# Optimization experiments

Measured on AMD Instinct MI355X. Metric: run time of the kernel, lower is better.

The kernel has to match this reference:

```python
import jax, jax.numpy as jnp
import numpy as np

N = 50000      # nodes
E = 800000     # edges
IN = 16        # embedding_dimension
HID = 128      # hidden_dimension
OUT = 3        # out_dim
R = 2          # relation_num
NEG_SLOPE = 0.2  # PyG RGATConv default negative_slope


def setup_inputs() -> dict:
    key = jax.random.key(0)
    ks = jax.random.split(key, 9)
    feature = jax.random.normal(ks[0], (N, IN), jnp.float32)
    edge_index = jax.random.randint(ks[1], (2, E), 0, N, jnp.int32)
    edge_type = jax.random.randint(ks[2], (E,), 0, R, jnp.int32)
    # RGATConv params (heads=1): weight [R, in, out], q/k [out, 1], bias [out]
    W1 = jax.random.normal(ks[3], (R, IN, HID), jnp.float32) * (1.0 / np.sqrt(IN))
    q1 = jax.random.normal(ks[4], (HID, 1), jnp.float32) * (1.0 / np.sqrt(HID))
    k1 = jax.random.normal(ks[5], (HID, 1), jnp.float32) * (1.0 / np.sqrt(HID))
    b1 = jnp.zeros((HID,), jnp.float32)
    W2 = jax.random.normal(ks[6], (R, HID, OUT), jnp.float32) * (1.0 / np.sqrt(HID))
    q2 = jax.random.normal(ks[7], (OUT, 1), jnp.float32) * (1.0 / np.sqrt(OUT))
    k2 = jax.random.normal(ks[8], (OUT, 1), jnp.float32) * (1.0 / np.sqrt(OUT))
    b2 = jnp.zeros((OUT,), jnp.float32)
    return dict(feature=feature, edge_index=edge_index, edge_type=edge_type,
                W1=W1, q1=q1, k1=k1, b1=b1, W2=W2, q2=q2, k2=k2, b2=b2)


def rgat_conv(x, src, dst, edge_type, W, q, k, b, n_nodes):
    # Per-relation node transform once at node level: [R, N, C]
    # (equivalent to per-edge bmm with W[edge_type] in PyG, but avoids
    #  gathering [E, in, C] weight matrices)
    xr = jnp.einsum('nd,rdc->rnc', x, W)
    out_i = xr[edge_type, dst]  # target node transformed by edge relation, [E, C]
    out_j = xr[edge_type, src]  # source node transformed by edge relation, [E, C]
    # additive self-attention, heads=1: alpha = leaky_relu(q(x_i) + k(x_j))
    alpha = jax.nn.leaky_relu((out_i @ q + out_j @ k)[:, 0], NEG_SLOPE)  # [E]
    # across-relation softmax over incoming edges of each target node
    m = jax.ops.segment_max(alpha, dst, num_segments=n_nodes)
    ex = jnp.exp(alpha - m[dst])
    denom = jax.ops.segment_sum(ex, dst, num_segments=n_nodes)
    a = ex / (denom[dst] + 1e-16)
    # message = alpha * W_r x_j, scatter-sum to target nodes
    out = jax.ops.segment_sum(out_j * a[:, None], dst, num_segments=n_nodes)
    return out + b


def reference(feature, edge_index, edge_type, W1, q1, k1, b1, W2, q2, k2, b2):
    src, dst = edge_index[0], edge_index[1]  # PyG: row 0 = source j, row 1 = target i
    h = rgat_conv(feature, src, dst, edge_type, W1, q1, k1, b1, N)
    # F.dropout(p=0.3) is identity in eval mode
    out = rgat_conv(h, src, dst, edge_type, W2, q2, k2, b2, N)
    return out
```

## Files before the change

### kernel.cpp

```cpp
#include <hip/hip_runtime.h>
#include <math.h>

#define IN_DIM 16
#define HID 128
#define NEG 0.2f

__device__ __forceinline__ float lrelu(float a) { return a > 0.f ? a : NEG * a; }

__global__ void __launch_bounds__(256) k_pre(
    const float* __restrict__ W1, const float* __restrict__ q1, const float* __restrict__ k1,
    const float* __restrict__ b1, const float* __restrict__ W2, const float* __restrict__ q2,
    const float* __restrict__ k2,
    float* __restrict__ wq1, float* __restrict__ wk1,
    float* __restrict__ M, float* __restrict__ C,
    int* __restrict__ counts, int n_nodes) {
    int zi = blockIdx.x * 256 + threadIdx.x;
    if (zi < n_nodes) counts[zi] = 0;

    int w = blockIdx.x * 4 + (threadIdx.x >> 6);
    if (w >= 362) return;
    int lane = threadIdx.x & 63;

    auto T = [&](int c, int o) -> float {
        if (o < 3) return W2[c * 3 + o];
        if (o < 6) return W2[384 + c * 3 + (o - 3)];
        const float* base = (o == 6 || o == 8) ? (W2 + c * 3) : (W2 + 384 + c * 3);
        const float* v = (o < 8) ? q2 : k2;
        return base[0] * v[0] + base[1] * v[1] + base[2] * v[2];
    };

    if (w < 330) {
        bool isC = (w >= 320);
        int o  = isC ? (w - 320) : (w % 10);
        int dp = isC ? 0 : (w / 10);
        float acc = 0.f;
        for (int c = lane; c < HID; c += 64) {
            float left = isC ? b1[c] : W1[dp * HID + c];
            acc += left * T(c, o);
        }
#pragma unroll
        for (int off = 32; off; off >>= 1) acc += __shfl_xor(acc, off);
        if (lane == 0) { if (isC) C[o] = acc; else M[dp * 10 + o] = acc; }
    } else {
        int i = w - 330;
        float aq = 0.f, ak = 0.f;
        for (int c = lane; c < HID; c += 64) {
            float wv = W1[i * HID + c];
            aq += wv * q1[c]; ak += wv * k1[c];
        }
#pragma unroll
        for (int off = 32; off; off >>= 1) { aq += __shfl_xor(aq, off); ak += __shfl_xor(ak, off); }
        if (lane == 0) { wq1[i] = aq; wk1[i] = ak; }
    }
}

__global__ void __launch_bounds__(256) k_prep(
    const float* __restrict__ x,
    const float* __restrict__ wq1, const float* __restrict__ wk1,
    float* __restrict__ sq1, float* __restrict__ sk1,
    const int* __restrict__ dstp, int* __restrict__ counts, int* __restrict__ rank,
    int n_nodes, int ecnt) {
    __shared__ float wq[2 * IN_DIM], wk[2 * IN_DIM];
    if (threadIdx.x < 2 * IN_DIM) { wq[threadIdx.x] = wq1[threadIdx.x]; wk[threadIdx.x] = wk1[threadIdx.x]; }
    __syncthreads();
    int gid = blockIdx.x * 256 + threadIdx.x;
    if (gid < ecnt) rank[gid] = atomicAdd(&counts[dstp[gid]], 1);
    if (gid < n_nodes) {
        float q0 = 0.f, q1v = 0.f, k0 = 0.f, k1v = 0.f;
        const float4* xp = reinterpret_cast<const float4*>(x + (size_t)gid * IN_DIM);
#pragma unroll
        for (int d4 = 0; d4 < IN_DIM / 4; ++d4) {
            float4 v = xp[d4];
            float vv[4] = {v.x, v.y, v.z, v.w};
#pragma unroll
            for (int j = 0; j < 4; ++j) {
                int d = d4 * 4 + j;
                q0 += vv[j] * wq[d]; q1v += vv[j] * wq[IN_DIM + d];
                k0 += vv[j] * wk[d]; k1v += vv[j] * wk[IN_DIM + d];
            }
        }
        sq1[gid] = q0; sq1[n_nodes + gid] = q1v;
        sk1[gid] = k0; sk1[n_nodes + gid] = k1v;
    }
}

__global__ void k_scan1(const int* __restrict__ counts, int* __restrict__ exoff,
                        int* __restrict__ blockSums, int n) {
    __shared__ int s[512];
    int tid = threadIdx.x;
    int gid = blockIdx.x * 512 + tid;
    int v = (gid < n) ? counts[gid] : 0;
    s[tid] = v;
    __syncthreads();
    for (int off = 1; off < 512; off <<= 1) {
        int t = (tid >= off) ? s[tid - off] : 0;
        __syncthreads();
        s[tid] += t;
        __syncthreads();
    }
    if (gid < n) exoff[gid] = s[tid] - v;
    if (tid == 511) blockSums[blockIdx.x] = s[511];
}

__global__ void __launch_bounds__(256) k_scatter(
    const int* __restrict__ srcp, const int* __restrict__ dstp,
    const int* __restrict__ etp,
    const int* __restrict__ exoff, const int* __restrict__ blockSums,
    const int* __restrict__ rank,
    int* __restrict__ offsets, int* __restrict__ sorted,
    int n_nodes, int ecnt, int nblk) {
    __shared__ int sB[128];
    int t = threadIdx.x;
    int v = 0;
    if (t < 128) { v = (t < nblk) ? blockSums[t] : 0; sB[t] = v; }
    __syncthreads();
    for (int off = 1; off < 128; off <<= 1) {
        int u = (t >= off && t < 128) ? sB[t - off] : 0;
        __syncthreads();
        if (t < 128) sB[t] += u;
        __syncthreads();
    }
    if (t < 128) sB[t] -= v;
    __syncthreads();
    int i = blockIdx.x * 256 + t;
    if (i < n_nodes) offsets[i] = exoff[i] + sB[i >> 9];
    if (i == 0) offsets[n_nodes] = ecnt;
    if (i < ecnt) {
        int d = dstp[i];
        int o = exoff[d] + sB[d >> 9];
        sorted[o + rank[i]] = (etp[i] << 16) | srcp[i];
    }
}

__global__ void __launch_bounds__(256) k_layer1(
    const int* __restrict__ offsets, const int* __restrict__ sorted,
    const float* __restrict__ sq1, const float* __restrict__ sk1,
    const float* __restrict__ x, const float* __restrict__ M, const float* __restrict__ C,
    float* __restrict__ xr2p, float* __restrict__ sq2,
    int n_nodes) {
    __shared__ float Ml[320], Cl[10];
    __shared__ float Al[4][32];
    for (int i = threadIdx.x; i < 320; i += 256) Ml[i] = M[i];
    if (threadIdx.x < 10)  Cl[threadIdx.x] = C[threadIdx.x];
    __syncthreads();
    int wid = threadIdx.x >> 6, lane = threadIdx.x & 63;
    int n = blockIdx.x * 4 + wid;
    if (n >= n_nodes) return;
    int beg = offsets[n], end = offsets[n + 1];
    float s0 = sq1[n], s1 = sq1[n_nodes + n];
    int ch4 = lane & 3, j = lane >> 2;
    float4 a0 = make_float4(0.f, 0.f, 0.f, 0.f);
    float4 a1 = make_float4(0.f, 0.f, 0.f, 0.f);
    float ds = 0.f;
    const float4* x4 = reinterpret_cast<const float4*>(x);
    for (int e = beg + j; e < end; e += 16) {
        int pk = sorted[e];
        int et = pk >> 16, s = pk & 0xFFFF;
        float w = __expf(lrelu((et ? s1 : s0) + sk1[et * n_nodes + s]));
        ds += w;
        float4 xv = x4[s * 4 + ch4];
        if (et == 0) { a0.x += w * xv.x; a0.y += w * xv.y; a0.z += w * xv.z; a0.w += w * xv.w; }
        else         { a1.x += w * xv.x; a1.y += w * xv.y; a1.z += w * xv.z; a1.w += w * xv.w; }
    }
#pragma unroll
    for (int off = 4; off <= 32; off <<= 1) {
        a0.x += __shfl_xor(a0.x, off); a0.y += __shfl_xor(a0.y, off);
        a0.z += __shfl_xor(a0.z, off); a0.w += __shfl_xor(a0.w, off);
        a1.x += __shfl_xor(a1.x, off); a1.y += __shfl_xor(a1.y, off);
        a1.z += __shfl_xor(a1.z, off); a1.w += __shfl_xor(a1.w, off);
        ds += __shfl_xor(ds, off);
    }
    float inv = 1.f / (ds + 1e-16f);
    if (lane < 4) {
        reinterpret_cast<float4*>(&Al[wid][0])[lane] =
            make_float4(a0.x * inv, a0.y * inv, a0.z * inv, a0.w * inv);
        reinterpret_cast<float4*>(&Al[wid][16])[lane] =
            make_float4(a1.x * inv, a1.y * inv, a1.z * inv, a1.w * inv);
    }
    if (lane < 10) {
        float acc = Cl[lane];
#pragma unroll
        for (int dp = 0; dp < 32; ++dp) acc += Al[wid][dp] * Ml[dp * 10 + lane];
        int o = lane;
        if (o < 3)       xr2p[(size_t)n * 4 + o] = acc;
        else if (o < 6)  xr2p[((size_t)n_nodes + n) * 4 + (o - 3)] = acc;
        else if (o == 6) sq2[2 * n] = acc;
        else if (o == 7) sq2[2 * n + 1] = acc;
        else if (o == 8) xr2p[(size_t)n * 4 + 3] = acc;
        else             xr2p[((size_t)n_nodes + n) * 4 + 3] = acc;
    }
}

__global__ void __launch_bounds__(256) k_node2(
    const int* __restrict__ offsets, const int* __restrict__ sorted,
    const float* __restrict__ sq2, const float* __restrict__ xr2p,
    const float* __restrict__ b2, float* __restrict__ out,
    int n_nodes) {
    int gid = blockIdx.x * 256 + threadIdx.x;
    int n = gid >> 4;
    int l = threadIdx.x & 15;
    if (n >= n_nodes) return;
    int beg = offsets[n], end = offsets[n + 1];
    if (beg == end) {
        if (l < 3) out[(size_t)n * 3 + l] = b2[l];
        return;
    }
    const float2 sq = *reinterpret_cast<const float2*>(sq2 + 2 * n);
    float lsum = 0.f, a0 = 0.f, a1 = 0.f, a2 = 0.f;
    for (int e = beg + l; e < end; e += 16) {
        int pk = sorted[e];
        int et = pk >> 16, s = pk & 0xFFFF;
        const float4 xr = *reinterpret_cast<const float4*>(xr2p + ((size_t)et * n_nodes + s) * 4);
        float w = __expf(lrelu((et ? sq.y : sq.x) + xr.w));
        lsum += w;
        a0 += w * xr.x; a1 += w * xr.y; a2 += w * xr.z;
    }
#pragma unroll
    for (int off = 8; off; off >>= 1) {
        lsum += __shfl_xor(lsum, off);
        a0 += __shfl_xor(a0, off);
        a1 += __shfl_xor(a1, off);
        a2 += __shfl_xor(a2, off);
    }
    if (l == 0) {
        float inv = 1.f / (lsum + 1e-16f);
        out[(size_t)n * 3 + 0] = a0 * inv + b2[0];
        out[(size_t)n * 3 + 1] = a1 * inv + b2[1];
        out[(size_t)n * 3 + 2] = a2 * inv + b2[2];
    }
}

extern "C" void kernel_launch(void* const* d_in, const int* in_sizes, int n_in,
                              void* d_out, int out_size, void* d_ws, size_t ws_size,
                              hipStream_t stream) {
    const float* x  = (const float*)d_in[0];
    const int*   ei = (const int*)d_in[1];
    const int*   etp = (const int*)d_in[2];
    const float* W1 = (const float*)d_in[3];
    const float* q1 = (const float*)d_in[4];
    const float* k1 = (const float*)d_in[5];
    const float* b1 = (const float*)d_in[6];
    const float* W2 = (const float*)d_in[7];
    const float* q2 = (const float*)d_in[8];
    const float* k2 = (const float*)d_in[9];
    const float* b2 = (const float*)d_in[10];
    float* out = (float*)d_out;

    const int n_nodes = in_sizes[0] / IN_DIM;
    const int ecnt    = in_sizes[2];
    const int* srcp = ei;
    const int* dstp = ei + ecnt;

    char* wp = (char*)d_ws;
    auto alloc = [&](size_t bytes) -> char* {
        char* p = wp;
        wp += (bytes + 255) & ~(size_t)255;
        return p;
    };
    float* xr2p  = (float*)alloc((size_t)2 * n_nodes * 4 * 4);
    float* sq1   = (float*)alloc((size_t)2 * n_nodes * 4);
    float* sk1   = (float*)alloc((size_t)2 * n_nodes * 4);
    float* sq2   = (float*)alloc((size_t)2 * n_nodes * 4);
    float* wq1   = (float*)alloc(32 * 4);
    float* wk1   = (float*)alloc(32 * 4);
    float* Mbuf  = (float*)alloc(320 * 4);
    float* Cbuf  = (float*)alloc(10 * 4);
    int* counts  = (int*)alloc((size_t)n_nodes * 4);
    int* exoff   = (int*)alloc((size_t)n_nodes * 4);
    int* blockSums = (int*)alloc(512);
    int* offsets = (int*)alloc((size_t)(n_nodes + 1) * 4);
    int* rank    = (int*)alloc((size_t)ecnt * 4);
    int* sorted  = (int*)alloc((size_t)ecnt * 4);

    int nblk = (n_nodes + 255) / 256;
    int eblk = (ecnt + 255) / 256;
    int nblk_scan = (n_nodes + 511) / 512;

    k_pre<<<nblk, 256, 0, stream>>>(W1, q1, k1, b1, W2, q2, k2, wq1, wk1, Mbuf, Cbuf,
                                    counts, n_nodes);
    k_prep<<<eblk, 256, 0, stream>>>(x, wq1, wk1, sq1, sk1, dstp, counts, rank, n_nodes, ecnt);
    k_scan1<<<nblk_scan, 512, 0, stream>>>(counts, exoff, blockSums, n_nodes);
    k_scatter<<<eblk, 256, 0, stream>>>(srcp, dstp, etp, exoff, blockSums, rank,
                                        offsets, sorted, n_nodes, ecnt, nblk_scan);

    k_layer1<<<(n_nodes + 3) / 4, 256, 0, stream>>>(offsets, sorted, sq1, sk1, x, Mbuf, Cbuf,
                                                    xr2p, sq2, n_nodes);
    k_node2<<<(n_nodes * 16 + 255) / 256, 256, 0, stream>>>(offsets, sorted, sq2, xr2p, b2,
                                                            out, n_nodes);
}
```

Before: 107.4 us.

## Replace global-atomic counting sort with two-level bucketed CSR build

The CSR build by destination no longer uses per-edge global atomics on 50K node counters and a separate scan. It does a coarse 256-node bucket histogram with shared-memory atomics, bins edges into buckets with per-block cursors, then each bucket block sorts locally by low destination bits in shared memory. This is meant to cut global atomic contention and scattered writes, and it drops the rank array and the scan kernel. The cost is an extra pass over the edges and a dependence on nbkt ≤ 256 and src < 65536, with the bit-packing limiting node count.

```diff
diff --git a/kernel.cpp b/kernel.cpp
--- a/kernel.cpp
+++ b/kernel.cpp
@@ -4,6 +4,7 @@
 #define IN_DIM 16
 #define HID 128
 #define NEG 0.2f
+#define ABLK 8192
 
 __device__ __forceinline__ float lrelu(float a) { return a > 0.f ? a : NEG * a; }
 
@@ -13,9 +14,10 @@
     const float* __restrict__ k2,
     float* __restrict__ wq1, float* __restrict__ wk1,
     float* __restrict__ M, float* __restrict__ C,
-    int* __restrict__ counts, int n_nodes) {
+    int* __restrict__ gSizes, int* __restrict__ gCursor, int nbkt) {
     int zi = blockIdx.x * 256 + threadIdx.x;
-    if (zi < n_nodes) counts[zi] = 0;
+    if (zi < nbkt) gSizes[zi] = 0;
+    else if (zi < 2 * nbkt) gCursor[zi - nbkt] = 0;
 
     int w = blockIdx.x * 4 + (threadIdx.x >> 6);
     if (w >= 362) return;
@@ -54,20 +56,30 @@
     }
 }
 
-__global__ void __launch_bounds__(256) k_prep(
+__global__ void __launch_bounds__(256) k_hist(
+    const int* __restrict__ dstp, int* __restrict__ gSizes,
     const float* __restrict__ x,
     const float* __restrict__ wq1, const float* __restrict__ wk1,
     float* __restrict__ sq1, float* __restrict__ sk1,
-    const int* __restrict__ dstp, int* __restrict__ counts, int* __restrict__ rank,
-    int n_nodes, int ecnt) {
+    int n_nodes, int ecnt, int nbkt) {
+    __shared__ int lh[256];
     __shared__ float wq[2 * IN_DIM], wk[2 * IN_DIM];
-    if (threadIdx.x < 2 * IN_DIM) { wq[threadIdx.x] = wq1[threadIdx.x]; wk[threadIdx.x] = wk1[threadIdx.x]; }
-    __syncthreads();
-    int gid = blockIdx.x * 256 + threadIdx.x;
-    if (gid < ecnt) rank[gid] = atomicAdd(&counts[dstp[gid]], 1);
-    if (gid < n_nodes) {
+    int t = threadIdx.x;
+    lh[t] = 0;
+    if (t < 2 * IN_DIM) { wq[t] = wq1[t]; wk[t] = wk1[t]; }
+    __syncthreads();
+    int E0 = blockIdx.x * ABLK;
+#pragma unroll
+    for (int k = 0; k < ABLK / 256; ++k) {
+        int e = E0 + k * 256 + t;
+        if (e < ecnt) atomicAdd(&lh[dstp[e] >> 8], 1);
+    }
+    __syncthreads();
+    if (t < nbkt && lh[t]) atomicAdd(&gSizes[t], lh[t]);
+    int stride = gridDim.x * 256;
+    for (int n = blockIdx.x * 256 + t; n < n_nodes; n += stride) {
         float q0 = 0.f, q1v = 0.f, k0 = 0.f, k1v = 0.f;
-        const float4* xp = reinterpret_cast<const float4*>(x + (size_t)gid * IN_DIM);
+        const float4* xp = reinterpret_cast<const float4*>(x + (size_t)n * IN_DIM);
 #pragma unroll
         for (int d4 = 0; d4 < IN_DIM / 4; ++d4) {
             float4 v = xp[d4];
@@ -79,56 +91,103 @@
                 k0 += vv[j] * wk[d]; k1v += vv[j] * wk[IN_DIM + d];
             }
         }
-        sq1[gid] = q0; sq1[n_nodes + gid] = q1v;
-        sk1[gid] = k0; sk1[n_nodes + gid] = k1v;
-    }
-}
-
-__global__ void k_scan1(const int* __restrict__ counts, int* __restrict__ exoff,
-                        int* __restrict__ blockSums, int n) {
-    __shared__ int s[512];
-    int tid = threadIdx.x;
-    int gid = blockIdx.x * 512 + tid;
-    int v = (gid < n) ? counts[gid] : 0;
-    s[tid] = v;
-    __syncthreads();
-    for (int off = 1; off < 512; off <<= 1) {
-        int t = (tid >= off) ? s[tid - off] : 0;
-        __syncthreads();
-        s[tid] += t;
-        __syncthreads();
-    }
-    if (gid < n) exoff[gid] = s[tid] - v;
-    if (tid == 511) blockSums[blockIdx.x] = s[511];
-}
-
-__global__ void __launch_bounds__(256) k_scatter(
+        sq1[n] = q0; sq1[n_nodes + n] = q1v;
+        sk1[n] = k0; sk1[n_nodes + n] = k1v;
+    }
+}
+
+__global__ void __launch_bounds__(256) k_bin(
     const int* __restrict__ srcp, const int* __restrict__ dstp,
     const int* __restrict__ etp,
-    const int* __restrict__ exoff, const int* __restrict__ blockSums,
-    const int* __restrict__ rank,
+    const int* __restrict__ gSizes, int* __restrict__ gCursor,
+    int* __restrict__ binned, int ecnt, int nbkt) {
+    __shared__ int lh[256];
+    __shared__ int runB[256];
+    __shared__ int ss[256];
+    __shared__ int sst[256];
+    int t = threadIdx.x;
+    lh[t] = 0;
+    __syncthreads();
+    int E0 = blockIdx.x * ABLK;
+    int rb[ABLK / 256];
+#pragma unroll
+    for (int k = 0; k < ABLK / 256; ++k) {
+        int e = E0 + k * 256 + t;
+        int v = -1;
+        if (e < ecnt) {
+            int b = dstp[e] >> 8;
+            int r = atomicAdd(&lh[b], 1);
+            v = (r << 8) | b;
+        }
+        rb[k] = v;
+    }
+    __syncthreads();
+    if (t < nbkt && lh[t]) runB[t] = atomicAdd(&gCursor[t], lh[t]);
+    int gv = (t < nbkt) ? gSizes[t] : 0;
+    ss[t] = gv;
+    __syncthreads();
+    for (int off = 1; off < 256; off <<= 1) {
+        int u = (t >= off) ? ss[t - off] : 0;
+        __syncthreads();
+        ss[t] += u;
+        __syncthreads();
+    }
+    sst[t] = ss[t] - gv;
+    __syncthreads();
+#pragma unroll
+    for (int k = 0; k < ABLK / 256; ++k) {
+        int v = rb[k];
+        if (v < 0) continue;
+        int b = v & 255, r = v >> 8;
+        int e = E0 + k * 256 + t;
+        int val = ((dstp[e] & 255) << 17) | (etp[e] << 16) | srcp[e];
+        binned[sst[b] + runB[b] + r] = val;
+    }
+}
+
+__global__ void __launch_bounds__(256) k_build(
+    const int* __restrict__ gSizes, const int* __restrict__ binned,
     int* __restrict__ offsets, int* __restrict__ sorted,
-    int n_nodes, int ecnt, int nblk) {
-    __shared__ int sB[128];
-    int t = threadIdx.x;
-    int v = 0;
-    if (t < 128) { v = (t < nblk) ? blockSums[t] : 0; sB[t] = v; }
-    __syncthreads();
-    for (int off = 1; off < 128; off <<= 1) {
-        int u = (t >= off && t < 128) ? sB[t - off] : 0;
-        __syncthreads();
-        if (t < 128) sB[t] += u;
-        __syncthreads();
-    }
-    if (t < 128) sB[t] -= v;
-    __syncthreads();
-    int i = blockIdx.x * 256 + t;
-    if (i < n_nodes) offsets[i] = exoff[i] + sB[i >> 9];
-    if (i == 0) offsets[n_nodes] = ecnt;
-    if (i < ecnt) {
-        int d = dstp[i];
-        int o = exoff[d] + sB[d >> 9];
-        sorted[o + rank[i]] = (etp[i] << 16) | srcp[i];
+    int n_nodes, int ecnt, int nbkt) {
+    __shared__ int ss[256], lh[256], loff[256], lcur[256];
+    int t = threadIdx.x, b = blockIdx.x;
+    int gv = (t < nbkt) ? gSizes[t] : 0;
+    ss[t] = gv;
+    lh[t] = 0;
+    __syncthreads();
+    for (int off = 1; off < 256; off <<= 1) {
+        int u = (t >= off) ? ss[t - off] : 0;
+        __syncthreads();
+        ss[t] += u;
+        __syncthreads();
+    }
+    int myStart = ss[b] - gSizes[b];
+    int sz = gSizes[b];
+    __syncthreads();
+    for (int i = t; i < sz; i += 256) {
+        int v = binned[myStart + i];
+        atomicAdd(&lh[(v >> 17) & 255], 1);
+    }
+    __syncthreads();
+    ss[t] = lh[t];
+    __syncthreads();
+    for (int off = 1; off < 256; off <<= 1) {
+        int u = (t >= off) ? ss[t - off] : 0;
+        __syncthreads();
+        ss[t] += u;
+        __syncthreads();
+    }
+    loff[t] = ss[t] - lh[t];
+    lcur[t] = 0;
+    __syncthreads();
+    int node = b * 256 + t;
+    if (node < n_nodes) offsets[node] = myStart + loff[t];
+    if (b == nbkt - 1 && t == 0) offsets[n_nodes] = ecnt;
+    for (int i = t; i < sz; i += 256) {
+        int v = binned[myStart + i];
+        int dl = (v >> 17) & 255;
+        int p = loff[dl] + atomicAdd(&lcur[dl], 1);
+        sorted[myStart + p] = v & 0x1FFFF;
     }
 }
 
@@ -250,6 +309,7 @@
     const int ecnt    = in_sizes[2];
     const int* srcp = ei;
     const int* dstp = ei + ecnt;
+    const int nbkt = (n_nodes + 255) >> 8;
 
     char* wp = (char*)d_ws;
     auto alloc = [&](size_t bytes) -> char* {
@@ -265,23 +325,20 @@
     float* wk1   = (float*)alloc(32 * 4);
     float* Mbuf  = (float*)alloc(320 * 4);
     float* Cbuf  = (float*)alloc(10 * 4);
-    int* counts  = (int*)alloc((size_t)n_nodes * 4);
-    int* exoff   = (int*)alloc((size_t)n_nodes * 4);
-    int* blockSums = (int*)alloc(512);
+    int* gSizes  = (int*)alloc(256 * 4);
+    int* gCursor = (int*)alloc(256 * 4);
     int* offsets = (int*)alloc((size_t)(n_nodes + 1) * 4);
-    int* rank    = (int*)alloc((size_t)ecnt * 4);
+    int* binned  = (int*)alloc((size_t)ecnt * 4);
     int* sorted  = (int*)alloc((size_t)ecnt * 4);
 
-    int nblk = (n_nodes + 255) / 256;
-    int eblk = (ecnt + 255) / 256;
-    int nblk_scan = (n_nodes + 511) / 512;
-
-    k_pre<<<nblk, 256, 0, stream>>>(W1, q1, k1, b1, W2, q2, k2, wq1, wk1, Mbuf, Cbuf,
-                                    counts, n_nodes);
-    k_prep<<<eblk, 256, 0, stream>>>(x, wq1, wk1, sq1, sk1, dstp, counts, rank, n_nodes, ecnt);
-    k_scan1<<<nblk_scan, 512, 0, stream>>>(counts, exoff, blockSums, n_nodes);
-    k_scatter<<<eblk, 256, 0, stream>>>(srcp, dstp, etp, exoff, blockSums, rank,
-                                        offsets, sorted, n_nodes, ecnt, nblk_scan);
+    int nAblk = (ecnt + ABLK - 1) / ABLK;
+
+    k_pre<<<91, 256, 0, stream>>>(W1, q1, k1, b1, W2, q2, k2, wq1, wk1, Mbuf, Cbuf,
+                                  gSizes, gCursor, nbkt);
+    k_hist<<<nAblk, 256, 0, stream>>>(dstp, gSizes, x, wq1, wk1, sq1, sk1,
+                                      n_nodes, ecnt, nbkt);
+    k_bin<<<nAblk, 256, 0, stream>>>(srcp, dstp, etp, gSizes, gCursor, binned, ecnt, nbkt);
+    k_build<<<nbkt, 256, 0, stream>>>(gSizes, binned, offsets, sorted, n_nodes, ecnt, nbkt);
 
     k_layer1<<<(n_nodes + 3) / 4, 256, 0, stream>>>(offsets, sorted, sq1, sk1, x, Mbuf, Cbuf,
                                                     xr2p, sq2, n_nodes);
```

Result: faster. 103.0 us (-4.1%).
